# Kernel tuning notes

Measured on AMD Instinct MI355X. Metric: run time of the kernel, lower is better.

Reference implementation:

```python
import jax, jax.numpy as jnp
import numpy as np


def setup_inputs() -> dict:
    key = jax.random.key(0)
    k = jax.random.split(key, 6)
    B, H, W, C = 16, 128, 128, 256
    NH, KD, VD = 8, 64, 64
    return {
        "key_value": jax.random.normal(k[0], (B, H, W, C), dtype=jnp.float32),
        "Wk": jax.random.normal(k[1], (C, NH * KD), dtype=jnp.float32) * (C ** -0.5),
        "bk": jnp.zeros((NH * KD,), dtype=jnp.float32),
        "Wv": jax.random.normal(k[2], (C, NH * VD), dtype=jnp.float32) * (C ** -0.5),
        "bv": jnp.zeros((NH * VD,), dtype=jnp.float32),
        "query": jax.random.normal(k[3], (1, 1, NH, KD), dtype=jnp.float32) * 0.05,
    }


def reference(key_value, Wk, bk, Wv, bv, query):
    B, H, W, C = key_value.shape
    _, _, NH, KD = query.shape
    VD = Wv.shape[1] // NH
    S = H * W  # flattened spatial length
    kv = key_value.reshape(B, S, C)
    # 1x1 conv == per-pixel dense projection
    k = (kv @ Wk + bk).reshape(B, S, NH, KD)   # [B,S,NH,KD]
    v = (kv @ Wv + bv).reshape(B, S, NH, VD)   # [B,S,NH,VD]
    # learned query dotted with keys (no sqrt scaling in original)
    scores = jnp.einsum("bshd,hd->bsh", k, query[0, 0])  # [B,S,NH]
    probs = jax.nn.softmax(scores, axis=1)                 # softmax over spatial axis
    out = jnp.einsum("bsh,bshd->bhd", probs, v)            # [B,NH,VD]
    return out
```

## Files before the change

kernel.cpp:

```cpp
#include <hip/hip_runtime.h>
#include <stdint.h>

typedef unsigned short u16;
typedef unsigned int u32;

typedef __attribute__((ext_vector_type(8))) __bf16 bf16x8;
typedef __attribute__((ext_vector_type(4))) float f32x4;

#define SDIM 16384
#define CDIM 256

__device__ __forceinline__ u16 f2bf(float f) {
    union { float f; u32 i; } v; v.f = f;
    u32 r = v.i + 0x7FFFu + ((v.i >> 16) & 1u);
    return (u16)(r >> 16);
}
__device__ __forceinline__ float bf_lo(u32 w) { union { u32 i; float f; } v; v.i = w << 16;        return v.f; }
__device__ __forceinline__ float bf_hi(u32 w) { union { u32 i; float f; } v; v.i = w & 0xFFFF0000u; return v.f; }

__global__ __launch_bounds__(256) void k_prep(const float* __restrict__ Wk,
                                              const float* __restrict__ bk,
                                              const float* __restrict__ q,
                                              u16* __restrict__ wqb_g,
                                              float* __restrict__ bq,
                                              float* __restrict__ zero_region) {
    int idx = blockIdx.x * 256 + threadIdx.x;
    int h = idx >> 8, c = idx & 255;
    float s = 0.f;
    if (h < 8) {
        const float4* wp = (const float4*)(Wk + (size_t)c * 512 + h * 64);
        const float4* qp = (const float4*)(q + h * 64);
        #pragma unroll
        for (int j = 0; j < 16; ++j) {
            float4 w = wp[j], qq = qp[j];
            s += w.x * qq.x + w.y * qq.y + w.z * qq.z + w.w * qq.w;
        }
    }
    wqb_g[h * 256 + c] = f2bf(s);
    if (idx < 8) {
        float sb = 0.f;
        for (int d = 0; d < 64; ++d) sb += bk[idx * 64 + d] * q[idx * 64 + d];
        bq[idx] = sb;
    }
    for (int j = idx; j < 32896; j += 4096) zero_region[j] = 0.f;
}

__global__ __launch_bounds__(256, 3) void k_main(const float* __restrict__ kv,
                                                 const u16* __restrict__ wqb_g,
                                                 const float* __restrict__ bq_g,
                                                 float* __restrict__ tglob,
                                                 float* __restrict__ zglob) {
    __shared__ u16 klds[64 * 264];
    __shared__ u16 wqb[16 * 264];
    __shared__ float pl[64 * 8];
    __shared__ float zp[4 * 8];

    const int t = threadIdx.x;
    const int lane = t & 63;
    const int wave = t >> 6;
    const int blk = blockIdx.x;
    const int b = blk >> 8;

    {
        int i0 = t, i1 = t + 256;
        int h0 = i0 >> 5, k0 = i0 & 31;
        int h1 = i1 >> 5, k1 = i1 & 31;
        *(uint4*)&wqb[h0 * 264 + k0 * 8] = *(const uint4*)&wqb_g[h0 * 256 + k0 * 8];
        *(uint4*)&wqb[h1 * 264 + k1 * 8] = *(const uint4*)&wqb_g[h1 * 256 + k1 * 8];
    }

    const float4* kvp = (const float4*)(kv + ((size_t)blk << 14));
    #pragma unroll
    for (int j = 0; j < 16; ++j) {
        int f = j * 256 + t;
        float4 g = kvp[f];
        uint2 w;
        w.x = (u32)f2bf(g.x) | ((u32)f2bf(g.y) << 16);
        w.y = (u32)f2bf(g.z) | ((u32)f2bf(g.w) << 16);
        *(uint2*)&klds[(f >> 6) * 264 + (f & 63) * 4] = w;
    }
    __syncthreads();

    const int h16 = lane & 15, q4 = lane >> 4;
    bf16x8 bfrag[8];
    #pragma unroll
    for (int ks = 0; ks < 8; ++ks) {
        uint4 r = *(const uint4*)&wqb[h16 * 264 + ks * 32 + q4 * 8];
        bfrag[ks] = __builtin_bit_cast(bf16x8, r);
    }
    const int px0 = wave * 16;
    f32x4 acc = {0.f, 0.f, 0.f, 0.f};
    #pragma unroll
    for (int ks = 0; ks < 8; ++ks) {
        uint4 r = *(const uint4*)&klds[(px0 + h16) * 264 + ks * 32 + q4 * 8];
        bf16x8 a = __builtin_bit_cast(bf16x8, r);
        acc = __builtin_amdgcn_mfma_f32_16x16x32_bf16(a, bfrag[ks], acc, 0, 0, 0);
    }
    float bqv = (h16 < 8) ? bq_g[h16] : 0.f;
    float e0 = __expf(acc[0] + bqv);
    float e1 = __expf(acc[1] + bqv);
    float e2 = __expf(acc[2] + bqv);
    float e3 = __expf(acc[3] + bqv);
    if (h16 < 8) {
        pl[(px0 + q4 * 4 + 0) * 8 + h16] = e0;
        pl[(px0 + q4 * 4 + 1) * 8 + h16] = e1;
        pl[(px0 + q4 * 4 + 2) * 8 + h16] = e2;
        pl[(px0 + q4 * 4 + 3) * 8 + h16] = e3;
    }
    float zv = e0 + e1 + e2 + e3;
    zv += __shfl_xor(zv, 16);
    zv += __shfl_xor(zv, 32);
    if (lane < 8) zp[wave * 8 + lane] = zv;
    __syncthreads();

    if (t < 8) atomicAdd(&zglob[b * 8 + t], zp[t] + zp[8 + t] + zp[16 + t] + zp[24 + t]);

    const int sg = t & 3, cg = t >> 2;
    float tac[32];
    #pragma unroll
    for (int i = 0; i < 32; ++i) tac[i] = 0.f;
    #pragma unroll 4
    for (int i = 0; i < 16; ++i) {
        int px = sg + i * 4;
        uint2 kw = *(const uint2*)&klds[px * 264 + cg * 4];
        float k0 = bf_lo(kw.x), k1 = bf_hi(kw.x);
        float k2 = bf_lo(kw.y), k3 = bf_hi(kw.y);
        float4 p0 = *(const float4*)&pl[px * 8];
        float4 p1 = *(const float4*)&pl[px * 8 + 4];
        float ph[8] = {p0.x, p0.y, p0.z, p0.w, p1.x, p1.y, p1.z, p1.w};
        #pragma unroll
        for (int h = 0; h < 8; ++h) {
            tac[h * 4 + 0] += k0 * ph[h];
            tac[h * 4 + 1] += k1 * ph[h];
            tac[h * 4 + 2] += k2 * ph[h];
            tac[h * 4 + 3] += k3 * ph[h];
        }
    }
    #pragma unroll
    for (int i = 0; i < 32; ++i) {
        tac[i] += __shfl_xor(tac[i], 1);
        tac[i] += __shfl_xor(tac[i], 2);
    }
    if (sg == 0) {
        float* tb = tglob + (size_t)b * 2048;
        #pragma unroll
        for (int h = 0; h < 8; ++h)
            #pragma unroll
            for (int k = 0; k < 4; ++k)
                atomicAdd(&tb[h * 256 + cg * 4 + k], tac[h * 4 + k]);
    }
}

__global__ __launch_bounds__(64) void k_out(const float* __restrict__ tglob,
                                            const float* __restrict__ zglob,
                                            const float* __restrict__ Wv,
                                            const float* __restrict__ bv,
                                            float* __restrict__ out) {
    int bh = blockIdx.x;
    int h = bh & 7, d = threadIdx.x;
    const float* tr = tglob + (size_t)bh * 256;
    const float* wv = Wv + h * 64 + d;
    float acc = 0.f;
    #pragma unroll 8
    for (int c = 0; c < 256; ++c)
        acc += tr[c] * wv[(size_t)c * 512];
    out[bh * 64 + d] = acc / zglob[bh] + bv[h * 64 + d];
}

extern "C" void kernel_launch(void* const* d_in, const int* in_sizes, int n_in,
                              void* d_out, int out_size, void* d_ws, size_t ws_size,
                              hipStream_t stream) {
    const float* kv = (const float*)d_in[0];
    const float* Wk = (const float*)d_in[1];
    const float* bk = (const float*)d_in[2];
    const float* Wv = (const float*)d_in[3];
    const float* bv = (const float*)d_in[4];
    const float* q  = (const float*)d_in[5];

    char* ws = (char*)d_ws;
    u16*   wqb_g = (u16*)(ws);
    float* bq    = (float*)(ws + 8192);
    float* tglob = (float*)(ws + 16384);
    float* zglob = (float*)(ws + 16384 + 131072);

    k_prep<<<16,   256, 0, stream>>>(Wk, bk, q, wqb_g, bq, tglob );
    k_main<<<4096, 256, 0, stream>>>(kv, wqb_g, bq, tglob, zglob);
    k_out <<<128,  64,  0, stream>>>(tglob, zglob, Wv, bv, (float*)d_out);
}
```

Baseline: 480.8 us.

## Loop four pixel tiles per block and replace atomics with per-block partials

Each k_main block now processes 256 pixels in four 64-pixel iterations, so the grid shrinks from 4096 to 1024 blocks. Instead of atomically accumulating into a zeroed global buffer, each block writes its own 2048-float partial and its z partial, and k_out reduces the 64 partials per batch. This removes contended float atomics and the zeroing pass. The cost is that the loop serialises load and compute within a block with no prefetch, and extra partial data has to be written and then read back.

```diff
diff --git a/kernel.cpp b/kernel.cpp
--- a/kernel.cpp
+++ b/kernel.cpp
@@ -22,8 +22,7 @@
                                               const float* __restrict__ bk,
                                               const float* __restrict__ q,
                                               u16* __restrict__ wqb_g,
-                                              float* __restrict__ bq,
-                                              float* __restrict__ zero_region) {
+                                              float* __restrict__ bq) {
     int idx = blockIdx.x * 256 + threadIdx.x;
     int h = idx >> 8, c = idx & 255;
     float s = 0.f;
@@ -42,14 +41,13 @@
         for (int d = 0; d < 64; ++d) sb += bk[idx * 64 + d] * q[idx * 64 + d];
         bq[idx] = sb;
     }
-    for (int j = idx; j < 32896; j += 4096) zero_region[j] = 0.f;
 }
 
 __global__ __launch_bounds__(256, 3) void k_main(const float* __restrict__ kv,
                                                  const u16* __restrict__ wqb_g,
                                                  const float* __restrict__ bq_g,
-                                                 float* __restrict__ tglob,
-                                                 float* __restrict__ zglob) {
+                                                 float* __restrict__ partials,
+                                                 float* __restrict__ zpart) {
     __shared__ u16 klds[64 * 264];
     __shared__ u16 wqb[16 * 264];
     __shared__ float pl[64 * 8];
@@ -59,7 +57,7 @@
     const int lane = t & 63;
     const int wave = t >> 6;
     const int blk = blockIdx.x;
-    const int b = blk >> 8;
+    const int b = blk >> 6, grp = blk & 63;
 
     {
         int i0 = t, i1 = t + 256;
@@ -68,17 +66,6 @@
         *(uint4*)&wqb[h0 * 264 + k0 * 8] = *(const uint4*)&wqb_g[h0 * 256 + k0 * 8];
         *(uint4*)&wqb[h1 * 264 + k1 * 8] = *(const uint4*)&wqb_g[h1 * 256 + k1 * 8];
     }
-
-    const float4* kvp = (const float4*)(kv + ((size_t)blk << 14));
-    #pragma unroll
-    for (int j = 0; j < 16; ++j) {
-        int f = j * 256 + t;
-        float4 g = kvp[f];
-        uint2 w;
-        w.x = (u32)f2bf(g.x) | ((u32)f2bf(g.y) << 16);
-        w.y = (u32)f2bf(g.z) | ((u32)f2bf(g.w) << 16);
-        *(uint2*)&klds[(f >> 6) * 264 + (f & 63) * 4] = w;
-    }
     __syncthreads();
 
     const int h16 = lane & 15, q4 = lane >> 4;
@@ -88,83 +75,125 @@
         uint4 r = *(const uint4*)&wqb[h16 * 264 + ks * 32 + q4 * 8];
         bfrag[ks] = __builtin_bit_cast(bf16x8, r);
     }
+    const float bqv = (h16 < 8) ? bq_g[h16] : 0.f;
     const int px0 = wave * 16;
-    f32x4 acc = {0.f, 0.f, 0.f, 0.f};
-    #pragma unroll
-    for (int ks = 0; ks < 8; ++ks) {
-        uint4 r = *(const uint4*)&klds[(px0 + h16) * 264 + ks * 32 + q4 * 8];
-        bf16x8 a = __builtin_bit_cast(bf16x8, r);
-        acc = __builtin_amdgcn_mfma_f32_16x16x32_bf16(a, bfrag[ks], acc, 0, 0, 0);
-    }
-    float bqv = (h16 < 8) ? bq_g[h16] : 0.f;
-    float e0 = __expf(acc[0] + bqv);
-    float e1 = __expf(acc[1] + bqv);
-    float e2 = __expf(acc[2] + bqv);
-    float e3 = __expf(acc[3] + bqv);
-    if (h16 < 8) {
-        pl[(px0 + q4 * 4 + 0) * 8 + h16] = e0;
-        pl[(px0 + q4 * 4 + 1) * 8 + h16] = e1;
-        pl[(px0 + q4 * 4 + 2) * 8 + h16] = e2;
-        pl[(px0 + q4 * 4 + 3) * 8 + h16] = e3;
-    }
-    float zv = e0 + e1 + e2 + e3;
-    zv += __shfl_xor(zv, 16);
-    zv += __shfl_xor(zv, 32);
-    if (lane < 8) zp[wave * 8 + lane] = zv;
-    __syncthreads();
-
-    if (t < 8) atomicAdd(&zglob[b * 8 + t], zp[t] + zp[8 + t] + zp[16 + t] + zp[24 + t]);
-
     const int sg = t & 3, cg = t >> 2;
+
     float tac[32];
     #pragma unroll
     for (int i = 0; i < 32; ++i) tac[i] = 0.f;
-    #pragma unroll 4
-    for (int i = 0; i < 16; ++i) {
-        int px = sg + i * 4;
-        uint2 kw = *(const uint2*)&klds[px * 264 + cg * 4];
-        float k0 = bf_lo(kw.x), k1 = bf_hi(kw.x);
-        float k2 = bf_lo(kw.y), k3 = bf_hi(kw.y);
-        float4 p0 = *(const float4*)&pl[px * 8];
-        float4 p1 = *(const float4*)&pl[px * 8 + 4];
-        float ph[8] = {p0.x, p0.y, p0.z, p0.w, p1.x, p1.y, p1.z, p1.w};
-        #pragma unroll
-        for (int h = 0; h < 8; ++h) {
-            tac[h * 4 + 0] += k0 * ph[h];
-            tac[h * 4 + 1] += k1 * ph[h];
-            tac[h * 4 + 2] += k2 * ph[h];
-            tac[h * 4 + 3] += k3 * ph[h];
-        }
-    }
+    float zacc = 0.f;
+
+    const size_t pixbase = (size_t)(b << 14) + grp * 256;
+
+    for (int it = 0; it < 4; ++it) {
+        const float4* kvp = (const float4*)(kv + (pixbase + it * 64) * CDIM);
+        #pragma unroll
+        for (int j = 0; j < 16; ++j) {
+            int f = j * 256 + t;
+            float4 g = kvp[f];
+            uint2 w;
+            w.x = (u32)f2bf(g.x) | ((u32)f2bf(g.y) << 16);
+            w.y = (u32)f2bf(g.z) | ((u32)f2bf(g.w) << 16);
+            *(uint2*)&klds[(f >> 6) * 264 + (f & 63) * 4] = w;
+        }
+        __syncthreads();
+
+        f32x4 acc = {0.f, 0.f, 0.f, 0.f};
+        #pragma unroll
+        for (int ks = 0; ks < 8; ++ks) {
+            uint4 r = *(const uint4*)&klds[(px0 + h16) * 264 + ks * 32 + q4 * 8];
+            bf16x8 a = __builtin_bit_cast(bf16x8, r);
+            acc = __builtin_amdgcn_mfma_f32_16x16x32_bf16(a, bfrag[ks], acc, 0, 0, 0);
+        }
+        float e0 = __expf(acc[0] + bqv);
+        float e1 = __expf(acc[1] + bqv);
+        float e2 = __expf(acc[2] + bqv);
+        float e3 = __expf(acc[3] + bqv);
+        if (h16 < 8) {
+            pl[(px0 + q4 * 4 + 0) * 8 + h16] = e0;
+            pl[(px0 + q4 * 4 + 1) * 8 + h16] = e1;
+            pl[(px0 + q4 * 4 + 2) * 8 + h16] = e2;
+            pl[(px0 + q4 * 4 + 3) * 8 + h16] = e3;
+        }
+        float zv = e0 + e1 + e2 + e3;
+        zv += __shfl_xor(zv, 16);
+        zv += __shfl_xor(zv, 32);
+        zacc += zv;
+        __syncthreads();
+
+        #pragma unroll 4
+        for (int i = 0; i < 16; ++i) {
+            int px = sg + i * 4;
+            uint2 kw = *(const uint2*)&klds[px * 264 + cg * 4];
+            float k0 = bf_lo(kw.x), k1 = bf_hi(kw.x);
+            float k2 = bf_lo(kw.y), k3 = bf_hi(kw.y);
+            float4 p0 = *(const float4*)&pl[px * 8];
+            float4 p1 = *(const float4*)&pl[px * 8 + 4];
+            float ph[8] = {p0.x, p0.y, p0.z, p0.w, p1.x, p1.y, p1.z, p1.w};
+            #pragma unroll
+            for (int h = 0; h < 8; ++h) {
+                tac[h * 4 + 0] += k0 * ph[h];
+                tac[h * 4 + 1] += k1 * ph[h];
+                tac[h * 4 + 2] += k2 * ph[h];
+                tac[h * 4 + 3] += k3 * ph[h];
+            }
+        }
+        __syncthreads();
+    }
+
+    if (lane < 8) zp[wave * 8 + lane] = zacc;
+    __syncthreads();
+    if (t < 8) zpart[blk * 8 + t] = zp[t] + zp[8 + t] + zp[16 + t] + zp[24 + t];
+
     #pragma unroll
     for (int i = 0; i < 32; ++i) {
         tac[i] += __shfl_xor(tac[i], 1);
         tac[i] += __shfl_xor(tac[i], 2);
     }
     if (sg == 0) {
-        float* tb = tglob + (size_t)b * 2048;
-        #pragma unroll
-        for (int h = 0; h < 8; ++h)
-            #pragma unroll
-            for (int k = 0; k < 4; ++k)
-                atomicAdd(&tb[h * 256 + cg * 4 + k], tac[h * 4 + k]);
-    }
-}
-
-__global__ __launch_bounds__(64) void k_out(const float* __restrict__ tglob,
-                                            const float* __restrict__ zglob,
-                                            const float* __restrict__ Wv,
-                                            const float* __restrict__ bv,
-                                            float* __restrict__ out) {
+        float* pb = partials + (size_t)blk * 2048;
+        #pragma unroll
+        for (int h = 0; h < 8; ++h) {
+            float4 v = {tac[h * 4 + 0], tac[h * 4 + 1], tac[h * 4 + 2], tac[h * 4 + 3]};
+            *(float4*)&pb[h * 256 + cg * 4] = v;
+        }
+    }
+}
+
+__global__ __launch_bounds__(256) void k_out(const float* __restrict__ partials,
+                                             const float* __restrict__ zpart,
+                                             const float* __restrict__ Wv,
+                                             const float* __restrict__ bv,
+                                             float* __restrict__ out) {
+    __shared__ float tlds[256];
+    __shared__ float zsh;
     int bh = blockIdx.x;
-    int h = bh & 7, d = threadIdx.x;
-    const float* tr = tglob + (size_t)bh * 256;
-    const float* wv = Wv + h * 64 + d;
-    float acc = 0.f;
+    int b = bh >> 3, h = bh & 7, t = threadIdx.x;
+
+    const float* p = partials + (size_t)(b * 64) * 2048 + h * 256 + t;
+    float s = 0.f;
     #pragma unroll 8
-    for (int c = 0; c < 256; ++c)
-        acc += tr[c] * wv[(size_t)c * 512];
-    out[bh * 64 + d] = acc / zglob[bh] + bv[h * 64 + d];
+    for (int j = 0; j < 64; ++j) s += p[(size_t)j * 2048];
+    tlds[t] = s;
+
+    if (t < 64) {
+        float zv = zpart[(b * 64 + t) * 8 + h];
+        #pragma unroll
+        for (int o = 32; o > 0; o >>= 1) zv += __shfl_xor(zv, o);
+        if (t == 0) zsh = zv;
+    }
+    __syncthreads();
+
+    if (t < 64) {
+        int d = t;
+        const float* wv = Wv + h * 64 + d;
+        float acc = 0.f;
+        #pragma unroll 8
+        for (int c = 0; c < 256; ++c)
+            acc += tlds[c] * wv[(size_t)c * 512];
+        out[bh * 64 + d] = acc / zsh + bv[h * 64 + d];
+    }
 }
 
 extern "C" void kernel_launch(void* const* d_in, const int* in_sizes, int n_in,
@@ -178,12 +207,12 @@
     const float* q  = (const float*)d_in[5];
 
     char* ws = (char*)d_ws;
-    u16*   wqb_g = (u16*)(ws);
-    float* bq    = (float*)(ws + 8192);
-    float* tglob = (float*)(ws + 16384);
-    float* zglob = (float*)(ws + 16384 + 131072);
-
-    k_prep<<<16,   256, 0, stream>>>(Wk, bk, q, wqb_g, bq, tglob );
-    k_main<<<4096, 256, 0, stream>>>(kv, wqb_g, bq, tglob, zglob);
-    k_out <<<128,  64,  0, stream>>>(tglob, zglob, Wv, bv, (float*)d_out);
-}
+    u16*   wqb_g    = (u16*)(ws);
+    float* bq       = (float*)(ws + 8192);
+    float* partials = (float*)(ws + 16384);
+    float* zpart    = (float*)(ws + 16384 + 8388608);
+
+    k_prep<<<16,   256, 0, stream>>>(Wk, bk, q, wqb_g, bq);
+    k_main<<<1024, 256, 0, stream>>>(kv, wqb_g, bq, partials, zpart);
+    k_out <<<128,  256, 0, stream>>>(partials, zpart, Wv, bv, (float*)d_out);
+}
```

Result: faster. 395.4 us (-17.8%).
